# Performance work log

Hardware: AMD Instinct MI355X
Metric: run time of the kernel (lower is better)

## Reference

```python
import jax, jax.numpy as jnp
import numpy as np

B, N, D, DK = 8, 2048, 1024, 64
GAMMA = 0.001

def setup_inputs() -> dict:
    key = jax.random.key(0)
    ks = jax.random.split(key, 6)
    x = jax.random.normal(ks[0], (B, N, D), dtype=jnp.float32)
    # nn.Linear weights are [out_features, in_features]; init std=gamma,
    # except fc1/fc2 (modules 4,5) which get std=1e-12 in the original.
    Wq = GAMMA * jax.random.normal(ks[1], (DK, D), dtype=jnp.float32)
    Wk = GAMMA * jax.random.normal(ks[2], (DK, D), dtype=jnp.float32)
    Wv = GAMMA * jax.random.normal(ks[3], (D, D), dtype=jnp.float32)
    W1 = 1e-12 * jax.random.normal(ks[4], (DK, D), dtype=jnp.float32)
    W2 = 1e-12 * jax.random.normal(ks[5], (D, DK), dtype=jnp.float32)
    return {"x": x, "Wq": Wq, "Wk": Wk, "Wv": Wv, "W1": W1, "W2": W2}

def reference(x, Wq, Wk, Wv, W1, W2):
    # Q,K: [B,N,DK]; V: [B,N,D]
    Q = jnp.einsum('bnd,kd->bnk', x, Wq)
    K = jnp.einsum('bnd,kd->bnk', x, Wk)
    V = jnp.einsum('bnd,ed->bne', x, Wv)
    # Linear (non-softmax) attention: (Q @ K^T) @ V
    scores = jnp.einsum('bnk,bmk->bnm', Q, K)      # [B,N,N]
    attention = jnp.einsum('bnm,bme->bne', scores, V)  # [B,N,D]
    x_skip = x + attention
    fc = jnp.einsum('bnd,kd->bnk', x_skip, W1)     # [B,N,DK]
    out = jnp.einsum('bnk,dk->bnd', fc, W2)        # [B,N,D]
    return out
```

## Files before the change

### kernel.cpp

```cpp
#include <hip/hip_runtime.h>

typedef __attribute__((ext_vector_type(8))) __bf16 bf16x8;
typedef __attribute__((ext_vector_type(4))) float f32x4;
typedef unsigned short u16;

#define MFMA16(a, b, c) __builtin_amdgcn_mfma_f32_16x16x32_bf16(a, b, c, 0, 0, 0)

__device__ __forceinline__ u16 f2bf(float f) {
    unsigned u = __float_as_uint(f);
    unsigned r = ((u >> 16) & 1u) + 0x7fffu;
    return (u16)((u + r) >> 16);
}
__device__ __forceinline__ float bf2f(u16 h) {
    return __uint_as_float(((unsigned)h) << 16);
}
__device__ __forceinline__ bf16x8 frag(const u16* base, int rtile, int lane, int kofs) {
    return *(const bf16x8*)(base + (rtile + (lane & 15)) * 72 + kofs + (lane >> 4) * 8);
}

__global__ __launch_bounds__(256) void qkf_kernel(
    const float* __restrict__ x, const float* __restrict__ Wq,
    const float* __restrict__ Wk, const float* __restrict__ W1,
    u16* __restrict__ Qb, u16* __restrict__ Kb, float* __restrict__ fcb)
{
    __shared__ __align__(16) u16 SM[6 * 4608];
    u16* Xh  = SM;
    u16* Xl  = SM + 4608;
    u16* Wqh = SM + 2 * 4608;
    u16* Wkh = SM + 3 * 4608;
    u16* W1h = SM + 4 * 4608;
    u16* W1l = SM + 5 * 4608;

    const int tid  = threadIdx.x;
    const int lane = tid & 63;
    const int wv   = tid >> 6;
    const int r0   = wv * 16;
    const long row0 = (long)blockIdx.x * 64;

    const f32x4 zero = {0.f, 0.f, 0.f, 0.f};
    f32x4 qa[4], ka[4], fa[4];
#pragma unroll
    for (int i = 0; i < 4; ++i) { qa[i] = zero; ka[i] = zero; fa[i] = zero; }

    const int sr = tid >> 4;
    const int sk = (tid & 15) * 4;

    float4 xv[4], qv[4], kv[4], w1v[4];
#define QKF_LOAD(K0)                                                          \
    {                                                                         \
        _Pragma("unroll")                                                     \
        for (int i = 0; i < 4; ++i) {                                         \
            int r = sr + i * 16;                                              \
            xv[i]  = *(const float4*)(x  + (row0 + r) * 1024 + (K0) + sk);    \
            qv[i]  = *(const float4*)(Wq + (long)r * 1024 + (K0) + sk);       \
            kv[i]  = *(const float4*)(Wk + (long)r * 1024 + (K0) + sk);       \
            w1v[i] = *(const float4*)(W1 + (long)r * 1024 + (K0) + sk);       \
        }                                                                     \
    }

    QKF_LOAD(0)
    for (int ch = 0; ch < 16; ++ch) {
        if (ch) __syncthreads();
#pragma unroll
        for (int i = 0; i < 4; ++i) {
            int r = sr + i * 16;
            ushort4 h, l;
            h.x = f2bf(xv[i].x); l.x = f2bf(xv[i].x - bf2f(h.x));
            h.y = f2bf(xv[i].y); l.y = f2bf(xv[i].y - bf2f(h.y));
            h.z = f2bf(xv[i].z); l.z = f2bf(xv[i].z - bf2f(h.z));
            h.w = f2bf(xv[i].w); l.w = f2bf(xv[i].w - bf2f(h.w));
            *(ushort4*)&Xh[r * 72 + sk] = h;
            *(ushort4*)&Xl[r * 72 + sk] = l;
            ushort4 hq;
            hq.x = f2bf(qv[i].x); hq.y = f2bf(qv[i].y);
            hq.z = f2bf(qv[i].z); hq.w = f2bf(qv[i].w);
            *(ushort4*)&Wqh[r * 72 + sk] = hq;
            ushort4 hk;
            hk.x = f2bf(kv[i].x); hk.y = f2bf(kv[i].y);
            hk.z = f2bf(kv[i].z); hk.w = f2bf(kv[i].w);
            *(ushort4*)&Wkh[r * 72 + sk] = hk;
            ushort4 hw, lw;
            hw.x = f2bf(w1v[i].x); lw.x = f2bf(w1v[i].x - bf2f(hw.x));
            hw.y = f2bf(w1v[i].y); lw.y = f2bf(w1v[i].y - bf2f(hw.y));
            hw.z = f2bf(w1v[i].z); lw.z = f2bf(w1v[i].z - bf2f(hw.z));
            hw.w = f2bf(w1v[i].w); lw.w = f2bf(w1v[i].w - bf2f(hw.w));
            *(ushort4*)&W1h[r * 72 + sk] = hw;
            *(ushort4*)&W1l[r * 72 + sk] = lw;
        }
        __syncthreads();
        if (ch < 15) QKF_LOAD((ch + 1) * 64)
#pragma unroll
        for (int kk = 0; kk < 64; kk += 32) {
            bf16x8 ah = frag(Xh, r0, lane, kk);
            bf16x8 al = frag(Xl, r0, lane, kk);
#pragma unroll
            for (int ct = 0; ct < 4; ++ct) {
                qa[ct] = MFMA16(ah, frag(Wqh, ct * 16, lane, kk), qa[ct]);
                ka[ct] = MFMA16(ah, frag(Wkh, ct * 16, lane, kk), ka[ct]);
                bf16x8 bh = frag(W1h, ct * 16, lane, kk);
                fa[ct] = MFMA16(ah, bh, fa[ct]);
                fa[ct] = MFMA16(al, bh, fa[ct]);
                fa[ct] = MFMA16(ah, frag(W1l, ct * 16, lane, kk), fa[ct]);
            }
        }
    }
#undef QKF_LOAD

    {
        int rr = r0 + (lane >> 4) * 4;
        int cc = lane & 15;
#pragma unroll
        for (int ct = 0; ct < 4; ++ct)
#pragma unroll
            for (int g = 0; g < 4; ++g)
                fcb[(row0 + rr + g) * 64 + ct * 16 + cc] = fa[ct][g];
    }
    float* rep = (float*)SM;
    for (int pass = 0; pass < 2; ++pass) {
        const f32x4* src = (pass == 0) ? qa : ka;
        u16* dst = (pass == 0) ? Qb : Kb;
        __syncthreads();
        int rr = r0 + (lane >> 4) * 4;
        int cc = lane & 15;
#pragma unroll
        for (int ct = 0; ct < 4; ++ct)
#pragma unroll
            for (int g = 0; g < 4; ++g)
                rep[(rr + g) * 65 + ct * 16 + cc] = src[ct][g];
        __syncthreads();
        int r = tid >> 2, c0 = (tid & 3) * 16;
        __align__(16) u16 tmp[16];
#pragma unroll
        for (int i = 0; i < 16; ++i) tmp[i] = f2bf(rep[r * 65 + c0 + i]);
        *(uint4*)(dst + (row0 + r) * 64 + c0) = *(uint4*)&tmp[0];
        *(uint4*)(dst + (row0 + r) * 64 + c0 + 8) = *(uint4*)&tmp[8];
    }
}

__global__ __launch_bounds__(256) void s_kernel(
    const u16* __restrict__ Kb, const float* __restrict__ x,
    float* __restrict__ Sp)
{
    __shared__ __align__(16) u16 Kt[64 * 72];
    __shared__ __align__(16) u16 Xt[64 * 72];

    const int tid = threadIdx.x, lane = tid & 63, wv = tid >> 6;
    const int dt = blockIdx.x, ks = blockIdx.y, b = blockIdx.z;
    const int n0 = ks * 256, d0 = dt * 64;

    const u16*   Kp = Kb + ((long)b * 2048 + n0) * 64;
    const float* xp = x  + ((long)b * 2048 + n0) * 1024 + d0;

    const f32x4 zero = {0.f, 0.f, 0.f, 0.f};
    f32x4 acc[4];
#pragma unroll
    for (int i = 0; i < 4; ++i) acc[i] = zero;

    uint4 kv0, kv1;
    float4 xv[4];
#define SK_LOAD(NB)                                                           \
    {                                                                         \
        kv0 = *(const uint4*)(Kp + (long)((NB) + lane) * 64 + wv * 16);       \
        kv1 = *(const uint4*)(Kp + (long)((NB) + lane) * 64 + wv * 16 + 8);   \
        _Pragma("unroll")                                                     \
        for (int i = 0; i < 4; ++i)                                           \
            xv[i] = *(const float4*)(xp + (long)((NB) + lane) * 1024 + wv * 16 + i * 4); \
    }

    SK_LOAD(0)
    for (int ch = 0; ch < 4; ++ch) {
        if (ch) __syncthreads();
#pragma unroll
        for (int i = 0; i < 8; ++i)
            Kt[(wv * 16 + i) * 72 + lane] = ((const u16*)&kv0)[i];
#pragma unroll
        for (int i = 0; i < 8; ++i)
            Kt[(wv * 16 + 8 + i) * 72 + lane] = ((const u16*)&kv1)[i];
#pragma unroll
        for (int i = 0; i < 4; ++i) {
            Xt[(wv * 16 + i * 4 + 0) * 72 + lane] = f2bf(xv[i].x);
            Xt[(wv * 16 + i * 4 + 1) * 72 + lane] = f2bf(xv[i].y);
            Xt[(wv * 16 + i * 4 + 2) * 72 + lane] = f2bf(xv[i].z);
            Xt[(wv * 16 + i * 4 + 3) * 72 + lane] = f2bf(xv[i].w);
        }
        __syncthreads();
        if (ch < 3) SK_LOAD((ch + 1) * 64)
#pragma unroll
        for (int kk = 0; kk < 64; kk += 32) {
            bf16x8 a = frag(Kt, wv * 16, lane, kk);
#pragma unroll
            for (int ct = 0; ct < 4; ++ct)
                acc[ct] = MFMA16(a, frag(Xt, ct * 16, lane, kk), acc[ct]);
        }
    }
#undef SK_LOAD

    float* C = Sp + ((long)ks * 8 + b) * 65536 + d0;
    const int rr = wv * 16 + (lane >> 4) * 4;
    const int cc = lane & 15;
#pragma unroll
    for (int ct = 0; ct < 4; ++ct)
#pragma unroll
        for (int g = 0; g < 4; ++g)
            C[(long)(rr + g) * 1024 + ct * 16 + cc] = acc[ct][g];
}

template <int AMODE, int BMODE, bool SPLIT, int ASLAB, int BSLAB, bool ACCUM>
__global__ __launch_bounds__(256) void mm_nt(
    const void* __restrict__ Ap, int lda, long bsA, long slabA,
    const void* __restrict__ Bp, int ldb, long bsB, long slabB,
    float* __restrict__ Cp, int ldc, long bsC, long splitC,
    int Kred, int nksplit)
{
    __shared__ __align__(16) u16 SMEM[(SPLIT ? 4 : 2) * 4608];
    u16* Ah = SMEM;
    u16* Bh = SMEM + 4608;
    u16* Al = SPLIT ? SMEM + 2 * 4608 : nullptr;
    u16* Bl = SPLIT ? SMEM + 3 * 4608 : nullptr;

    const int tid = threadIdx.x, lane = tid & 63, wv = tid >> 6;
    const int bm = blockIdx.x, bn = blockIdx.y;
    const int batch = blockIdx.z / nksplit;
    const int ks = blockIdx.z % nksplit;
    const int Kper = Kred / nksplit;
    const long kOff = (long)ks * Kper;

    const int r4 = tid >> 4, k4 = (tid & 15) * 4;
    const int r8 = tid >> 3, k8 = (tid & 7) * 8;

    const f32x4 zero = {0.f, 0.f, 0.f, 0.f};
    f32x4 acc[4];
#pragma unroll
    for (int i = 0; i < 4; ++i) acc[i] = zero;

    float4 fva[4], fvb[4];
    uint4  uva[2], uvb[2];

#define MM_LOADA(K0)                                                          \
    if constexpr (AMODE == 0) {                                               \
        const float* A = (const float*)Ap + (long)batch * bsA                 \
                       + (long)bm * 64 * lda + (K0);                          \
        _Pragma("unroll")                                                     \
        for (int i = 0; i < 4; ++i) {                                         \
            const float* p = A + (long)(r4 + i * 16) * lda + k4;              \
            float4 v = *(const float4*)p;                                     \
            _Pragma("unroll")                                                 \
            for (int s = 1; s < ASLAB; ++s) {                                 \
                float4 w = *(const float4*)(p + (long)s * slabA);             \
                v.x += w.x; v.y += w.y; v.z += w.z; v.w += w.w;               \
            }                                                                 \
            fva[i] = v;                                                       \
        }                                                                     \
    } else {                                                                  \
        const u16* A = (const u16*)Ap + (long)batch * bsA                     \
                     + (long)bm * 64 * lda + (K0);                            \
        _Pragma("unroll")                                                     \
        for (int i = 0; i < 2; ++i)                                           \
            uva[i] = *(const uint4*)(A + (long)(r8 + i * 32) * lda + k8);     \
    }
#define MM_LOADB(K0)                                                          \
    if constexpr (BMODE == 0) {                                               \
        const float* Bq = (const float*)Bp + (long)batch * bsB                \
                        + (long)bn * 64 * ldb + (K0);                         \
        _Pragma("unroll")                                                     \
        for (int i = 0; i < 4; ++i) {                                         \
            const float* p = Bq + (long)(r4 + i * 16) * ldb + k4;             \
            float4 v = *(const float4*)p;                                     \
            _Pragma("unroll")                                                 \
            for (int s = 1; s < BSLAB; ++s) {                                 \
                float4 w = *(const float4*)(p + (long)s * slabB);             \
                v.x += w.x; v.y += w.y; v.z += w.z; v.w += w.w;               \
            }                                                                 \
            fvb[i] = v;                                                       \
        }                                                                     \
    } else {                                                                  \
        const u16* Bq = (const u16*)Bp + (long)batch * bsB                    \
                      + (long)bn * 64 * ldb + (K0);                           \
        _Pragma("unroll")                                                     \
        for (int i = 0; i < 2; ++i)                                           \
            uvb[i] = *(const uint4*)(Bq + (long)(r8 + i * 32) * ldb + k8);    \
    }

    MM_LOADA(kOff) MM_LOADB(kOff)
    for (int k0 = 0; k0 < Kper; k0 += 64) {
        if (k0) __syncthreads();
        if constexpr (AMODE == 0) {
#pragma unroll
            for (int i = 0; i < 4; ++i) {
                int r = r4 + i * 16;
                ushort4 h;
                h.x = f2bf(fva[i].x); h.y = f2bf(fva[i].y);
                h.z = f2bf(fva[i].z); h.w = f2bf(fva[i].w);
                *(ushort4*)&Ah[r * 72 + k4] = h;
                if constexpr (SPLIT) {
                    ushort4 l;
                    l.x = f2bf(fva[i].x - bf2f(h.x)); l.y = f2bf(fva[i].y - bf2f(h.y));
                    l.z = f2bf(fva[i].z - bf2f(h.z)); l.w = f2bf(fva[i].w - bf2f(h.w));
                    *(ushort4*)&Al[r * 72 + k4] = l;
                }
            }
        } else {
#pragma unroll
            for (int i = 0; i < 2; ++i)
                *(uint4*)&Ah[(r8 + i * 32) * 72 + k8] = uva[i];
        }
        if constexpr (BMODE == 0) {
#pragma unroll
            for (int i = 0; i < 4; ++i) {
                int r = r4 + i * 16;
                ushort4 h;
                h.x = f2bf(fvb[i].x); h.y = f2bf(fvb[i].y);
                h.z = f2bf(fvb[i].z); h.w = f2bf(fvb[i].w);
                *(ushort4*)&Bh[r * 72 + k4] = h;
                if constexpr (SPLIT) {
                    ushort4 l;
                    l.x = f2bf(fvb[i].x - bf2f(h.x)); l.y = f2bf(fvb[i].y - bf2f(h.y));
                    l.z = f2bf(fvb[i].z - bf2f(h.z)); l.w = f2bf(fvb[i].w - bf2f(h.w));
                    *(ushort4*)&Bl[r * 72 + k4] = l;
                }
            }
        } else {
#pragma unroll
            for (int i = 0; i < 2; ++i)
                *(uint4*)&Bh[(r8 + i * 32) * 72 + k8] = uvb[i];
        }
        __syncthreads();
        if (k0 + 64 < Kper) { MM_LOADA(kOff + k0 + 64) MM_LOADB(kOff + k0 + 64) }
#pragma unroll
        for (int kk = 0; kk < 64; kk += 32) {
            bf16x8 ah = frag(Ah, wv * 16, lane, kk);
            bf16x8 al;
            if constexpr (SPLIT) al = frag(Al, wv * 16, lane, kk);
#pragma unroll
            for (int ct = 0; ct < 4; ++ct) {
                bf16x8 bh = frag(Bh, ct * 16, lane, kk);
                acc[ct] = MFMA16(ah, bh, acc[ct]);
                if constexpr (SPLIT) {
                    acc[ct] = MFMA16(al, bh, acc[ct]);
                    acc[ct] = MFMA16(ah, frag(Bl, ct * 16, lane, kk), acc[ct]);
                }
            }
        }
    }
#undef MM_LOADA
#undef MM_LOADB

    float* C = Cp + (long)batch * bsC + (long)ks * splitC
             + (long)bm * 64 * ldc + (long)bn * 64;
    const int rr = wv * 16 + (lane >> 4) * 4;
    const int cc = lane & 15;
#pragma unroll
    for (int ct = 0; ct < 4; ++ct)
#pragma unroll
        for (int g = 0; g < 4; ++g) {
            long idx = (long)(rr + g) * ldc + ct * 16 + cc;
            if constexpr (ACCUM) C[idx] += acc[ct][g];
            else                 C[idx] = acc[ct][g];
        }
}

extern "C" void kernel_launch(void* const* d_in, const int* in_sizes, int n_in,
                              void* d_out, int out_size, void* d_ws, size_t ws_size,
                              hipStream_t stream)
{
    const float* x  = (const float*)d_in[0];
    const float* Wq = (const float*)d_in[1];
    const float* Wk = (const float*)d_in[2];
    const float* Wv = (const float*)d_in[3];
    const float* W1 = (const float*)d_in[4];
    const float* W2 = (const float*)d_in[5];
    float* out = (float*)d_out;

    const size_t QB = 2097152, KBY = 2097152, FCB = 4194304,
                 SPB = 16777216, MBY = 8388608, PBB = 2097152;
    const size_t need = QB + KBY + FCB + SPB + MBY + PBB;

    u16 *Qb, *Kb;
    float *fcb, *Sp, *Mp, *PBp;
    if (ws_size >= need) {
        char* w = (char*)d_ws;
        Qb  = (u16*)w;    w += QB;
        Kb  = (u16*)w;    w += KBY;
        fcb = (float*)w;  w += FCB;
        Sp  = (float*)w;  w += SPB;
        Mp  = (float*)w;  w += MBY;
        PBp = (float*)w;
    } else {
        char* o = (char*)d_out;
        Qb  = (u16*)o;    o += QB;
        Kb  = (u16*)o;    o += KBY;
        Sp  = (float*)o;  o += SPB;
        Mp  = (float*)o;  o += MBY;
        PBp = (float*)o;
        fcb = (float*)d_ws;
    }

    qkf_kernel<<<dim3(256), 256, 0, stream>>>(x, Wq, Wk, W1, Qb, Kb, fcb);

    s_kernel<<<dim3(16, 8, 8), 256, 0, stream>>>(Kb, x, Sp);

    mm_nt<0, 0, false, 8, 1, false><<<dim3(1, 16, 32), 256, 0, stream>>>(
        Sp, 1024, 65536L, 524288L,   Wv, 1024, 0, 0,
        Mp, 1024, 65536L, 524288L, 1024, 4);

    mm_nt<0, 0, false, 1, 4, false><<<dim3(1, 1, 128), 256, 0, stream>>>(
        W1, 1024, 0, 0,   Mp, 1024, 65536L, 524288L,
        PBp, 64, 4096L, 32768L, 1024, 16);

    mm_nt<1, 0, false, 1, 16, true><<<dim3(32, 1, 8), 256, 0, stream>>>(
        Qb, 64, 131072L, 0,   PBp, 64, 4096L, 32768L,
        fcb, 64, 131072L, 0, 64, 1);

    mm_nt<0, 0, true, 1, 1, false><<<dim3(256, 16, 1), 256, 0, stream>>>(
        fcb, 64, 0, 0,   W2, 64, 0, 0,
        out, 1024, 0, 0, 64, 1);
}
```

Baseline: 220.4 us.

## Reassociate W1·Wv product, split-K QKF projection, and fuse partial-slab reductions

Instead of computing M = S·Wv per batch (an N×D×D-scale product) and then W1·M, the code now forms G = W1·Wv once (a 64×1024×1024 product) and contracts G with the per-batch S slabs. This removes the large per-batch matmul. The QKF projection is split across two K-halves (blockIdx.y) that write fp32 partial slabs. The downstream kernels add those slabs: s_kernel sums the two K partials, and the final mm sums the Q slabs and the fc partials via a new CSLAB epilogue. This adds fp32 workspace traffic in place of bf16 Q/K, and brings a strided scalar transposed B-load path for the new G product.

```diff
diff --git a/kernel.cpp b/kernel.cpp
--- a/kernel.cpp
+++ b/kernel.cpp
@@ -21,7 +21,7 @@
 __global__ __launch_bounds__(256) void qkf_kernel(
     const float* __restrict__ x, const float* __restrict__ Wq,
     const float* __restrict__ Wk, const float* __restrict__ W1,
-    u16* __restrict__ Qb, u16* __restrict__ Kb, float* __restrict__ fcb)
+    float* __restrict__ Qp, float* __restrict__ Kp, float* __restrict__ fcp)
 {
     __shared__ __align__(16) u16 SM[6 * 4608];
     u16* Xh  = SM;
@@ -36,6 +36,8 @@
     const int wv   = tid >> 6;
     const int r0   = wv * 16;
     const long row0 = (long)blockIdx.x * 64;
+    const int kb   = blockIdx.y * 512;
+    const long sOf = (long)blockIdx.y * 1048576;
 
     const f32x4 zero = {0.f, 0.f, 0.f, 0.f};
     f32x4 qa[4], ka[4], fa[4];
@@ -58,8 +60,8 @@
         }                                                                     \
     }
 
-    QKF_LOAD(0)
-    for (int ch = 0; ch < 16; ++ch) {
+    QKF_LOAD(kb)
+    for (int ch = 0; ch < 8; ++ch) {
         if (ch) __syncthreads();
 #pragma unroll
         for (int i = 0; i < 4; ++i) {
@@ -88,7 +90,7 @@
             *(ushort4*)&W1l[r * 72 + sk] = lw;
         }
         __syncthreads();
-        if (ch < 15) QKF_LOAD((ch + 1) * 64)
+        if (ch < 7) QKF_LOAD(kb + (ch + 1) * 64)
 #pragma unroll
         for (int kk = 0; kk < 64; kk += 32) {
             bf16x8 ah = frag(Xh, r0, lane, kk);
@@ -106,39 +108,21 @@
     }
 #undef QKF_LOAD
 
-    {
-        int rr = r0 + (lane >> 4) * 4;
-        int cc = lane & 15;
-#pragma unroll
-        for (int ct = 0; ct < 4; ++ct)
-#pragma unroll
-            for (int g = 0; g < 4; ++g)
-                fcb[(row0 + rr + g) * 64 + ct * 16 + cc] = fa[ct][g];
-    }
-    float* rep = (float*)SM;
-    for (int pass = 0; pass < 2; ++pass) {
-        const f32x4* src = (pass == 0) ? qa : ka;
-        u16* dst = (pass == 0) ? Qb : Kb;
-        __syncthreads();
-        int rr = r0 + (lane >> 4) * 4;
-        int cc = lane & 15;
-#pragma unroll
-        for (int ct = 0; ct < 4; ++ct)
-#pragma unroll
-            for (int g = 0; g < 4; ++g)
-                rep[(rr + g) * 65 + ct * 16 + cc] = src[ct][g];
-        __syncthreads();
-        int r = tid >> 2, c0 = (tid & 3) * 16;
-        __align__(16) u16 tmp[16];
-#pragma unroll
-        for (int i = 0; i < 16; ++i) tmp[i] = f2bf(rep[r * 65 + c0 + i]);
-        *(uint4*)(dst + (row0 + r) * 64 + c0) = *(uint4*)&tmp[0];
-        *(uint4*)(dst + (row0 + r) * 64 + c0 + 8) = *(uint4*)&tmp[8];
-    }
+    const int rr = r0 + (lane >> 4) * 4;
+    const int cc = lane & 15;
+#pragma unroll
+    for (int ct = 0; ct < 4; ++ct)
+#pragma unroll
+        for (int g = 0; g < 4; ++g) {
+            long o = sOf + (row0 + rr + g) * 64 + ct * 16 + cc;
+            Qp[o]  = qa[ct][g];
+            Kp[o]  = ka[ct][g];
+            fcp[o] = fa[ct][g];
+        }
 }
 
 __global__ __launch_bounds__(256) void s_kernel(
-    const u16* __restrict__ Kb, const float* __restrict__ x,
+    const float* __restrict__ Kp, const float* __restrict__ x,
     float* __restrict__ Sp)
 {
     __shared__ __align__(16) u16 Kt[64 * 72];
@@ -148,7 +132,7 @@
     const int dt = blockIdx.x, ks = blockIdx.y, b = blockIdx.z;
     const int n0 = ks * 256, d0 = dt * 64;
 
-    const u16*   Kp = Kb + ((long)b * 2048 + n0) * 64;
+    const float* Kq = Kp + ((long)b * 2048 + n0) * 64;
     const float* xp = x  + ((long)b * 2048 + n0) * 1024 + d0;
 
     const f32x4 zero = {0.f, 0.f, 0.f, 0.f};
@@ -156,28 +140,28 @@
 #pragma unroll
     for (int i = 0; i < 4; ++i) acc[i] = zero;
 
-    uint4 kv0, kv1;
-    float4 xv[4];
+    float4 kf[4], xv[4];
 #define SK_LOAD(NB)                                                           \
     {                                                                         \
-        kv0 = *(const uint4*)(Kp + (long)((NB) + lane) * 64 + wv * 16);       \
-        kv1 = *(const uint4*)(Kp + (long)((NB) + lane) * 64 + wv * 16 + 8);   \
-        _Pragma("unroll")                                                     \
-        for (int i = 0; i < 4; ++i)                                           \
+        _Pragma("unroll")                                                     \
+        for (int i = 0; i < 4; ++i) {                                         \
+            float4 a = *(const float4*)(Kq + (long)((NB) + lane) * 64 + wv * 16 + i * 4); \
+            float4 c = *(const float4*)(Kq + 1048576 + (long)((NB) + lane) * 64 + wv * 16 + i * 4); \
+            kf[i].x = a.x + c.x; kf[i].y = a.y + c.y;                         \
+            kf[i].z = a.z + c.z; kf[i].w = a.w + c.w;                         \
             xv[i] = *(const float4*)(xp + (long)((NB) + lane) * 1024 + wv * 16 + i * 4); \
+        }                                                                     \
     }
 
     SK_LOAD(0)
     for (int ch = 0; ch < 4; ++ch) {
         if (ch) __syncthreads();
 #pragma unroll
-        for (int i = 0; i < 8; ++i)
-            Kt[(wv * 16 + i) * 72 + lane] = ((const u16*)&kv0)[i];
-#pragma unroll
-        for (int i = 0; i < 8; ++i)
-            Kt[(wv * 16 + 8 + i) * 72 + lane] = ((const u16*)&kv1)[i];
-#pragma unroll
         for (int i = 0; i < 4; ++i) {
+            Kt[(wv * 16 + i * 4 + 0) * 72 + lane] = f2bf(kf[i].x);
+            Kt[(wv * 16 + i * 4 + 1) * 72 + lane] = f2bf(kf[i].y);
+            Kt[(wv * 16 + i * 4 + 2) * 72 + lane] = f2bf(kf[i].z);
+            Kt[(wv * 16 + i * 4 + 3) * 72 + lane] = f2bf(kf[i].w);
             Xt[(wv * 16 + i * 4 + 0) * 72 + lane] = f2bf(xv[i].x);
             Xt[(wv * 16 + i * 4 + 1) * 72 + lane] = f2bf(xv[i].y);
             Xt[(wv * 16 + i * 4 + 2) * 72 + lane] = f2bf(xv[i].z);
@@ -205,11 +189,12 @@
             C[(long)(rr + g) * 1024 + ct * 16 + cc] = acc[ct][g];
 }
 
-template <int AMODE, int BMODE, bool SPLIT, int ASLAB, int BSLAB, bool ACCUM>
+template <int AMODE, int BMODE, bool SPLIT, int ASLAB, int BSLAB, int CSLAB>
 __global__ __launch_bounds__(256) void mm_nt(
     const void* __restrict__ Ap, int lda, long bsA, long slabA,
     const void* __restrict__ Bp, int ldb, long bsB, long slabB,
     float* __restrict__ Cp, int ldc, long bsC, long splitC,
+    const float* __restrict__ Cin, long slabCin,
     int Kred, int nksplit)
 {
     __shared__ __align__(16) u16 SMEM[(SPLIT ? 4 : 2) * 4608];
@@ -235,6 +220,7 @@
 
     float4 fva[4], fvb[4];
     uint4  uva[2], uvb[2];
+    float  tvb[16];
 
 #define MM_LOADA(K0)                                                          \
     if constexpr (AMODE == 0) {                                               \
@@ -273,12 +259,18 @@
             }                                                                 \
             fvb[i] = v;                                                       \
         }                                                                     \
-    } else {                                                                  \
+    } else if constexpr (BMODE == 1) {                                        \
         const u16* Bq = (const u16*)Bp + (long)batch * bsB                    \
                       + (long)bn * 64 * ldb + (K0);                           \
         _Pragma("unroll")                                                     \
         for (int i = 0; i < 2; ++i)                                           \
             uvb[i] = *(const uint4*)(Bq + (long)(r8 + i * 32) * ldb + k8);    \
+    } else {                                                                  \
+        const float* Bq = (const float*)Bp + (long)batch * bsB                \
+                        + (long)(K0) * ldb + (long)bn * 64;                   \
+        _Pragma("unroll")                                                     \
+        for (int i = 0; i < 16; ++i)                                          \
+            tvb[i] = Bq[(long)((tid >> 6) + i * 4) * ldb + (tid & 63)];       \
     }
 
     MM_LOADA(kOff) MM_LOADB(kOff)
@@ -319,10 +311,14 @@
                     *(ushort4*)&Bl[r * 72 + k4] = l;
                 }
             }
-        } else {
+        } else if constexpr (BMODE == 1) {
 #pragma unroll
             for (int i = 0; i < 2; ++i)
                 *(uint4*)&Bh[(r8 + i * 32) * 72 + k8] = uvb[i];
+        } else {
+#pragma unroll
+            for (int i = 0; i < 16; ++i)
+                Bh[(tid & 63) * 72 + (tid >> 6) + i * 4] = f2bf(tvb[i]);
         }
         __syncthreads();
         if (k0 + 64 < Kper) { MM_LOADA(kOff + k0 + 64) MM_LOADB(kOff + k0 + 64) }
@@ -345,8 +341,8 @@
 #undef MM_LOADA
 #undef MM_LOADB
 
-    float* C = Cp + (long)batch * bsC + (long)ks * splitC
-             + (long)bm * 64 * ldc + (long)bn * 64;
+    const long coff = (long)batch * bsC + (long)bm * 64 * ldc + (long)bn * 64;
+    float* C = Cp + coff + (long)ks * splitC;
     const int rr = wv * 16 + (lane >> 4) * 4;
     const int cc = lane & 15;
 #pragma unroll
@@ -354,8 +350,13 @@
 #pragma unroll
         for (int g = 0; g < 4; ++g) {
             long idx = (long)(rr + g) * ldc + ct * 16 + cc;
-            if constexpr (ACCUM) C[idx] += acc[ct][g];
-            else                 C[idx] = acc[ct][g];
+            float v = acc[ct][g];
+            if constexpr (CSLAB > 0) {
+                const float* Ci = Cin + coff + idx;
+#pragma unroll
+                for (int s = 0; s < CSLAB; ++s) v += Ci[(long)s * slabCin];
+            }
+            C[idx] = v;
         }
 }
 
@@ -371,47 +372,48 @@
     const float* W2 = (const float*)d_in[5];
     float* out = (float*)d_out;
 
-    const size_t QB = 2097152, KBY = 2097152, FCB = 4194304,
-                 SPB = 16777216, MBY = 8388608, PBB = 2097152;
-    const size_t need = QB + KBY + FCB + SPB + MBY + PBB;
-
-    u16 *Qb, *Kb;
-    float *fcb, *Sp, *Mp, *PBp;
+    const size_t QPB = 8388608, KPB = 8388608, FCPB = 8388608,
+                 SPB = 16777216, GPB = 2097152, PBB = 2097152, FCB = 4194304;
+    const size_t need = QPB + KPB + FCPB + SPB + GPB + PBB + FCB;
+
+    float *Qp, *Kp, *fcp, *Sp, *Gp, *PBp, *fcb;
     if (ws_size >= need) {
         char* w = (char*)d_ws;
-        Qb  = (u16*)w;    w += QB;
-        Kb  = (u16*)w;    w += KBY;
-        fcb = (float*)w;  w += FCB;
+        Qp  = (float*)w;  w += QPB;
+        Kp  = (float*)w;  w += KPB;
+        fcp = (float*)w;  w += FCPB;
         Sp  = (float*)w;  w += SPB;
-        Mp  = (float*)w;  w += MBY;
-        PBp = (float*)w;
+        Gp  = (float*)w;  w += GPB;
+        PBp = (float*)w;  w += PBB;
+        fcb = (float*)w;
     } else {
         char* o = (char*)d_out;
-        Qb  = (u16*)o;    o += QB;
-        Kb  = (u16*)o;    o += KBY;
+        Qp  = (float*)o;  o += QPB;
+        Kp  = (float*)o;  o += KPB;
+        fcp = (float*)o;  o += FCPB;
         Sp  = (float*)o;  o += SPB;
-        Mp  = (float*)o;  o += MBY;
+        Gp  = (float*)o;  o += GPB;
         PBp = (float*)o;
         fcb = (float*)d_ws;
     }
 
-    qkf_kernel<<<dim3(256), 256, 0, stream>>>(x, Wq, Wk, W1, Qb, Kb, fcb);
-
-    s_kernel<<<dim3(16, 8, 8), 256, 0, stream>>>(Kb, x, Sp);
-
-    mm_nt<0, 0, false, 8, 1, false><<<dim3(1, 16, 32), 256, 0, stream>>>(
-        Sp, 1024, 65536L, 524288L,   Wv, 1024, 0, 0,
-        Mp, 1024, 65536L, 524288L, 1024, 4);
-
-    mm_nt<0, 0, false, 1, 4, false><<<dim3(1, 1, 128), 256, 0, stream>>>(
-        W1, 1024, 0, 0,   Mp, 1024, 65536L, 524288L,
-        PBp, 64, 4096L, 32768L, 1024, 16);
-
-    mm_nt<1, 0, false, 1, 16, true><<<dim3(32, 1, 8), 256, 0, stream>>>(
-        Qb, 64, 131072L, 0,   PBp, 64, 4096L, 32768L,
-        fcb, 64, 131072L, 0, 64, 1);
-
-    mm_nt<0, 0, true, 1, 1, false><<<dim3(256, 16, 1), 256, 0, stream>>>(
+    qkf_kernel<<<dim3(256, 2), 256, 0, stream>>>(x, Wq, Wk, W1, Qp, Kp, fcp);
+
+    s_kernel<<<dim3(16, 8, 8), 256, 0, stream>>>(Kp, x, Sp);
+
+    mm_nt<0, 2, false, 1, 1, 0><<<dim3(1, 16, 8), 256, 0, stream>>>(
+        W1, 1024, 0, 0,   Wv, 1024, 0, 0,
+        Gp, 1024, 0, 65536L, nullptr, 0, 1024, 8);
+
+    mm_nt<0, 0, false, 8, 8, 0><<<dim3(1, 1, 128), 256, 0, stream>>>(
+        Gp, 1024, 0, 65536L,   Sp, 1024, 65536L, 524288L,
+        PBp, 64, 4096L, 32768L, nullptr, 0, 1024, 16);
+
+    mm_nt<0, 0, false, 2, 16, 2><<<dim3(32, 1, 8), 256, 0, stream>>>(
+        Qp, 64, 131072L, 1048576L,   PBp, 64, 4096L, 32768L,
+        fcb, 64, 131072L, 0, fcp, 1048576L, 64, 1);
+
+    mm_nt<0, 0, true, 1, 1, 0><<<dim3(256, 16, 1), 256, 0, stream>>>(
         fcb, 64, 0, 0,   W2, 64, 0, 0,
-        out, 1024, 0, 0, 64, 1);
-}
+        out, 1024, 0, 0, nullptr, 0, 64, 1);
+}
```

Result: faster. 207.0 us (-6.1%).
